# Kernel optimization log

Measured on AMD Instinct MI355X. Metric: run time of the kernel, lower is better.

Reference implementation:

```python
import jax, jax.numpy as jnp
import numpy as np

S, T, B = 120, 10, 128          # sentence len, word len, batch
E, HW, HS = 80, 75, 700         # embedding, word-GRU hidden, sentence-GRU hidden
V = 30000                       # vocab size


def gru_scan(x, Wih, Whh, bih, bhh):
    """Single-direction GRU (PyTorch gate math). x: [T, N, in] -> (ys [T,N,H], h_T [N,H])."""
    H = Whh.shape[-1]
    xw = jnp.einsum('tni,gi->tng', x, Wih) + bih  # precompute input gates [T,N,3H]

    def step(h, xw_t):
        gh = h @ Whh.T + bhh
        r = jax.nn.sigmoid(xw_t[..., :H] + gh[..., :H])
        z = jax.nn.sigmoid(xw_t[..., H:2 * H] + gh[..., H:2 * H])
        n = jnp.tanh(xw_t[..., 2 * H:] + r * gh[..., 2 * H:])
        h_new = (1.0 - z) * n + z * h
        return h_new, h_new

    h0 = jnp.zeros((x.shape[1], H), x.dtype)
    hT, ys = jax.lax.scan(step, h0, xw)
    return ys, hT


def bigru_layer(x, Wih, Whh, bih, bhh):
    """Bidirectional GRU layer; params have leading dir axis [2,...]."""
    yf, hf = gru_scan(x, Wih[0], Whh[0], bih[0], bhh[0])
    yb, hb = gru_scan(x[::-1], Wih[1], Whh[1], bih[1], bhh[1])
    y = jnp.concatenate([yf, yb[::-1]], axis=-1)
    return y, hf, hb


def setup_inputs() -> dict:
    key = jax.random.key(0)
    ks = iter(jax.random.split(key, 40))

    def p(shape):
        return jax.random.normal(next(ks), shape, jnp.float32) * 0.05

    inp = {'x': jax.random.randint(next(ks), (S, T, B), 0, V)}
    inp['emb'] = p((V, E))
    # word encoder: 2-layer bi-GRU, layer0 in=E, layer1 in=2*HW
    inp['we_Wih0'] = p((2, 3 * HW, E)); inp['we_Whh0'] = p((2, 3 * HW, HW))
    inp['we_bih0'] = p((2, 3 * HW)); inp['we_bhh0'] = p((2, 3 * HW))
    inp['we_Wih1'] = p((2, 3 * HW, 2 * HW)); inp['we_Whh1'] = p((2, 3 * HW, HW))
    inp['we_bih1'] = p((2, 3 * HW)); inp['we_bhh1'] = p((2, 3 * HW))
    # sentence encoder: 2-layer bi-GRU, layer0 in=4*HW=300, layer1 in=2*HS
    inp['se_Wih0'] = p((2, 3 * HS, 4 * HW)); inp['se_Whh0'] = p((2, 3 * HS, HS))
    inp['se_bih0'] = p((2, 3 * HS)); inp['se_bhh0'] = p((2, 3 * HS))
    inp['se_Wih1'] = p((2, 3 * HS, 2 * HS)); inp['se_Whh1'] = p((2, 3 * HS, HS))
    inp['se_bih1'] = p((2, 3 * HS)); inp['se_bhh1'] = p((2, 3 * HS))
    return inp


def reference(x, emb,
              we_Wih0, we_Whh0, we_bih0, we_bhh0,
              we_Wih1, we_Whh1, we_bih1, we_bhh1,
              se_Wih0, se_Whh0, se_bih0, se_bhh0,
              se_Wih1, se_Whh1, se_bih1, se_bhh1):
    # Fold the python loop over 120 sentence positions into the batch:
    # x [S,T,B] -> [T, S*B]
    xt = jnp.transpose(x, (1, 0, 2)).reshape(T, S * B)
    xe = emb[xt]  # [T, S*B, E]
    y0, hf0, hb0 = bigru_layer(xe, we_Wih0, we_Whh0, we_bih0, we_bhh0)
    _, hf1, hb1 = bigru_layer(y0, we_Wih1, we_Whh1, we_bih1, we_bhh1)
    # torch h stacking: [l0_fwd, l0_bwd, l1_fwd, l1_bwd] concat on feature dim
    words = jnp.concatenate([hf0, hb0, hf1, hb1], axis=-1)  # [S*B, 4*HW]
    words = words.reshape(S, B, 4 * HW)
    y0s, sf0, sb0 = bigru_layer(words, se_Wih0, se_Whh0, se_bih0, se_bhh0)
    _, sf1, sb1 = bigru_layer(y0s, se_Wih1, se_Whh1, se_bih1, se_bhh1)
    h = jnp.concatenate([sf0, sb0, sf1, sb1], axis=-1)[None]  # [1, B, 4*HS]
    return h
```

## Files before the change

kernel.cpp:

```cpp
#include <hip/hip_runtime.h>
#include <hip/hip_bf16.h>

typedef __hip_bfloat16 bf16;
typedef __attribute__((ext_vector_type(8))) short bf16x8;
typedef __attribute__((ext_vector_type(4))) short bf16x4;
typedef __attribute__((ext_vector_type(4))) float f32x4;

__device__ __forceinline__ void stC(float* p, float v) { *p = v; }
__device__ __forceinline__ void stC(bf16* p, float v)  { *p = __float2bfloat16(v); }

__device__ __forceinline__ short f2s(float f) {
    bf16 b = __float2bfloat16(f);
    return __builtin_bit_cast(short, b);
}

__device__ __forceinline__ void gload16(const void* gp, void* lp) {
    __builtin_amdgcn_global_load_lds(
        (const __attribute__((address_space(1))) void*)gp,
        (__attribute__((address_space(3))) void*)lp, 16, 0, 0);
}

__device__ __forceinline__ float sigm(float x) {
    x = fminf(fmaxf(x, -40.f), 40.f);
    return 1.f / (1.f + expf(-x));
}
__device__ __forceinline__ float tanh_s(float x) {
    x = fminf(fmaxf(x, -20.f), 20.f);
    float e = expf(2.f * x);
    return 1.f - 2.f / (e + 1.f);
}

__device__ __forceinline__ bf16x8 ld8(const bf16* p) {
    return *reinterpret_cast<const bf16x8*>(p);
}
__device__ __forceinline__ bf16x8 ld8(const float* p) {
    const float4 f0 = *reinterpret_cast<const float4*>(p);
    const float4 f1 = *reinterpret_cast<const float4*>(p + 4);
    bf16x8 v;
    v[0] = f2s(f0.x); v[1] = f2s(f0.y); v[2] = f2s(f0.z); v[3] = f2s(f0.w);
    v[4] = f2s(f1.x); v[5] = f2s(f1.y); v[6] = f2s(f1.z); v[7] = f2s(f1.w);
    return v;
}
__device__ __forceinline__ bf16x8 ld8_8B(const bf16* p) {
    bf16x4 lo = *reinterpret_cast<const bf16x4*>(p);
    bf16x4 hi = *reinterpret_cast<const bf16x4*>(p + 4);
    bf16x8 v;
    v[0] = lo[0]; v[1] = lo[1]; v[2] = lo[2]; v[3] = lo[3];
    v[4] = hi[0]; v[5] = hi[1]; v[6] = hi[2]; v[7] = hi[3];
    return v;
}

__global__ void f2b(const float* __restrict__ src, bf16* __restrict__ dst, long n) {
    long i = (long)blockIdx.x * 256 + threadIdx.x;
    if (i < n) dst[i] = __float2bfloat16(src[i]);
}
__global__ void f2bpad(const float* __restrict__ src, bf16* __restrict__ dst,
                       int rows, int Ks, int Kd) {
    long i = (long)blockIdx.x * 256 + threadIdx.x;
    if (i >= (long)rows * Kd) return;
    int c = i % Kd; long r = i / Kd;
    dst[i] = __float2bfloat16(c < Ks ? src[r * Ks + c] : 0.f);
}
__global__ void f2bremap(const float* __restrict__ src, bf16* __restrict__ dst, int rows) {
    long i = (long)blockIdx.x * 256 + threadIdx.x;
    if (i >= (long)rows * 160) return;
    int c = i % 160; long r = i / 160;
    float v = 0.f;
    if (c < 75) v = src[r * 150 + c];
    else if (c >= 80 && c < 155) v = src[r * 150 + c - 5];
    dst[i] = __float2bfloat16(v);
}

#define MBM 128
#define MBN 64
#define MLD 40

__global__ __launch_bounds__(256) void gemm_mfma(
    const float* __restrict__ A, long sAd,
    const float* __restrict__ W, long sWd,
    bf16* __restrict__ C, long sCd,
    int M, int Nc, int K)
{
    __shared__ bf16 As[MBM * MLD];
    __shared__ bf16 Ws[MBN * MLD];
    const int d = blockIdx.z;
    A += (long)d * sAd; W += (long)d * sWd; C += (long)d * sCd;
    const int m0 = blockIdx.y * MBM;
    const int n0 = blockIdx.x * MBN;
    const int tid = threadIdx.x;
    const int w = tid >> 6, l = tid & 63;
    const int lr = l & 15, lq = l >> 4;

    f32x4 acc[2][4] = {};
    for (int k0 = 0; k0 < K; k0 += 32) {
#pragma unroll
        for (int i = 0; i < 2; ++i) {
            int u = tid + i * 256;
            int r = u >> 2, kk = (u & 3) * 8;
            bf16x8 v = {};
            if (m0 + r < M && k0 + kk < K)
                v = ld8(A + (long)(m0 + r) * K + k0 + kk);
            *reinterpret_cast<bf16x8*>(&As[r * MLD + kk]) = v;
        }
        {
            int r = tid >> 2, kk = (tid & 3) * 8;
            bf16x8 v = {};
            if (n0 + r < Nc && k0 + kk < K)
                v = ld8(W + (long)(n0 + r) * K + k0 + kk);
            *reinterpret_cast<bf16x8*>(&Ws[r * MLD + kk]) = v;
        }
        __syncthreads();
        bf16x8 af[2], bw[4];
        af[0] = *reinterpret_cast<const bf16x8*>(&As[(w * 32 + lr) * MLD + lq * 8]);
        af[1] = *reinterpret_cast<const bf16x8*>(&As[(w * 32 + 16 + lr) * MLD + lq * 8]);
#pragma unroll
        for (int ni = 0; ni < 4; ++ni)
            bw[ni] = *reinterpret_cast<const bf16x8*>(&Ws[(ni * 16 + lr) * MLD + lq * 8]);
#pragma unroll
        for (int mi = 0; mi < 2; ++mi)
#pragma unroll
            for (int ni = 0; ni < 4; ++ni)
                acc[mi][ni] = __builtin_amdgcn_mfma_f32_16x16x32_bf16(
                    af[mi], bw[ni], acc[mi][ni], 0, 0, 0);
        __syncthreads();
    }
#pragma unroll
    for (int mi = 0; mi < 2; ++mi)
#pragma unroll
        for (int reg = 0; reg < 4; ++reg) {
            int m = m0 + w * 32 + mi * 16 + lq * 4 + reg;
            if (m >= M) continue;
#pragma unroll
            for (int ni = 0; ni < 4; ++ni) {
                int n = n0 + ni * 16 + lr;
                if (n < Nc) stC(&C[(long)m * Nc + n], acc[mi][ni][reg]);
            }
        }
}

__global__ __launch_bounds__(256) void gemm_bt(
    const bf16* __restrict__ A, long sAd,
    const bf16* __restrict__ W, long sWd,
    bf16* __restrict__ C, long sCd,
    int M, int Nc, int KP)
{
    __shared__ bf16 As[128 * 64];
    __shared__ bf16 Ws[128 * 64];
    const int d = blockIdx.z;
    A += (long)d * sAd; W += (long)d * sWd; C += (long)d * sCd;
    const int nx = (Nc + 127) >> 7, ny = M >> 7;
    int id = blockIdx.x;
    int band = id / (8 * ny);
    int rr = id - band * 8 * ny;
    int bwd = nx - band * 8; if (bwd > 8) bwd = 8;
    const int bx = band * 8 + rr % bwd;
    const int by = rr / bwd;
    const int m0 = by << 7;
    const int n0 = bx << 7;
    const int tid = threadIdx.x;
    const int w = tid >> 6, l = tid & 63;
    const int lr = l & 15, lq = l >> 4;

    const int sr = tid >> 3;
    const int sg = tid & 7;
    const bf16x8 z8 = {};
    bf16x8 ra[4], rb[4];
    auto stage = [&](int k0) {
        const bool kin = (k0 + sg * 8) < KP;
#pragma unroll
        for (int i = 0; i < 4; ++i)
            ra[i] = kin ? ld8(A + (long)(m0 + sr + i * 32) * KP + k0 + sg * 8) : z8;
#pragma unroll
        for (int i = 0; i < 4; ++i)
            rb[i] = kin ? ld8(W + (long)(n0 + sr + i * 32) * KP + k0 + sg * 8) : z8;
    };

    f32x4 acc[2][8] = {};
    stage(0);
    for (int k0 = 0; k0 < KP; k0 += 64) {
#pragma unroll
        for (int i = 0; i < 4; ++i) {
            const int r = sr + i * 32;
            const int g = sg ^ (r & 7);
            *reinterpret_cast<bf16x8*>(&As[r * 64 + g * 8]) = ra[i];
            *reinterpret_cast<bf16x8*>(&Ws[r * 64 + g * 8]) = rb[i];
        }
        __syncthreads();
        if (k0 + 64 < KP) stage(k0 + 64);
#pragma unroll
        for (int ks = 0; ks < 2; ++ks) {
            const int gb = ks * 4 + lq;
            bf16x8 af[2], bw8[8];
#pragma unroll
            for (int mi = 0; mi < 2; ++mi) {
                const int r = w * 32 + mi * 16 + lr;
                af[mi] = *reinterpret_cast<const bf16x8*>(
                    &As[r * 64 + (gb ^ (r & 7)) * 8]);
            }
#pragma unroll
            for (int ni = 0; ni < 8; ++ni) {
                const int r = ni * 16 + lr;
                bw8[ni] = *reinterpret_cast<const bf16x8*>(
                    &Ws[r * 64 + (gb ^ (r & 7)) * 8]);
            }
#pragma unroll
            for (int mi = 0; mi < 2; ++mi)
#pragma unroll
                for (int ni = 0; ni < 8; ++ni)
                    acc[mi][ni] = __builtin_amdgcn_mfma_f32_16x16x32_bf16(
                        af[mi], bw8[ni], acc[mi][ni], 0, 0, 0);
        }
        __syncthreads();
    }
#pragma unroll
    for (int mi = 0; mi < 2; ++mi)
#pragma unroll
        for (int reg = 0; reg < 4; ++reg) {
            int m = m0 + w * 32 + mi * 16 + lq * 4 + reg;
#pragma unroll
            for (int ni = 0; ni < 8; ++ni) {
                int n = n0 + ni * 16 + lr;
                if (n < Nc) C[(long)m * Nc + n] = __float2bfloat16(acc[mi][ni][reg]);
            }
        }
}

#define NKS 22
#define HBPE (2 * 128 * 700)

struct StepJob {
    const bf16* Whh;
    const bf16* xw;
    const float* bih;
    const float* bhh;
    float* h;
    const bf16* hr;
    bf16* hw;
    bf16* y;
    const bf16* zb;
    int te0, te1;
    int tl0, tl1;
};

__global__ __launch_bounds__(512) void gru_step_sent2(StepJob ja, StepJob jb, int Cbuf)
{
    extern __shared__ bf16 Wlds[];
    const StepJob J = blockIdx.y ? jb : ja;
    const int jt = blockIdx.x, d = blockIdx.z;
    const int tid = threadIdx.x;
    const int w = tid >> 6, l = tid & 63;
    const int lr = l & 15, lq = l >> 4;
    const int j0c = jt * 16;
    const int jcol = j0c + lr;
    const bool jok = jcol < 700;

    const bf16* Wd = J.Whh + (long)d * 2100 * 700;
    {
        const int row = j0c + lr;
        const int kof = lq * 8;
#pragma unroll
        for (int i = 0; i < 9; ++i) {
            const int issue = w + i * 8;
            if (issue < 66) {
                const int g = issue % 3;
                const int kk = issue / 3;
                const bf16* src = (row < 700)
                    ? Wd + (long)(g * 700 + row) * 700 + kk * 32 + kof
                    : J.zb;
                gload16(src, &Wlds[(long)issue * 512]);
            }
        }
    }

    const int arow = w * 16 + lr;
    const bf16* Ab = J.hr + ((long)d * 128 + arow) * 700;
    bf16x8 areg[NKS];
#pragma unroll
    for (int kk = 0; kk < NKS; ++kk) {
        const int kb = kk * 32 + lq * 8;
        if (kb + 8 <= 700) {
            areg[kk] = ld8_8B(Ab + kb);
        } else {
            bf16x8 v = {};
            bf16x4 lo = *reinterpret_cast<const bf16x4*>(Ab + kb);
            v[0] = lo[0]; v[1] = lo[1]; v[2] = lo[2]; v[3] = lo[3];
            areg[kk] = v;
        }
    }

    const int te = d ? J.te1 : J.te0;
    const int tl = d ? J.tl1 : J.tl0;
    const bf16* xbase = J.xw + ((long)d * Cbuf + tl) * 128 * 2100;
    bf16 xg[3][4];
#pragma unroll
    for (int reg = 0; reg < 4; ++reg) {
        const int m = w * 16 + lq * 4 + reg;
        const bf16* xp = xbase + (long)m * 2100 + jcol;
#pragma unroll
        for (int g = 0; g < 3; ++g) xg[g][reg] = jok ? xp[g * 700] : bf16(0.f);
    }
    const int jc = jok ? jcol : 699;
    const float bir = J.bih[d * 2100 + jc];
    const float biz = J.bih[d * 2100 + 700 + jc];
    const float bin = J.bih[d * 2100 + 1400 + jc];
    const float bhr = J.bhh[d * 2100 + jc];
    const float bhz = J.bhh[d * 2100 + 700 + jc];
    const float bhn = J.bhh[d * 2100 + 1400 + jc];

    __syncthreads();

    f32x4 acc[3] = {};
#pragma unroll
    for (int kk = 0; kk < NKS; ++kk)
#pragma unroll
        for (int g = 0; g < 3; ++g) {
            bf16x8 b = *reinterpret_cast<const bf16x8*>(&Wlds[((kk * 3 + g) * 64 + l) * 8]);
            acc[g] = __builtin_amdgcn_mfma_f32_16x16x32_bf16(areg[kk], b, acc[g], 0, 0, 0);
        }

    if (jok) {
#pragma unroll
        for (int reg = 0; reg < 4; ++reg) {
            const int m = w * 16 + lq * 4 + reg;
            float r  = sigm((float)xg[0][reg] + bir + acc[0][reg] + bhr);
            float z  = sigm((float)xg[1][reg] + biz + acc[1][reg] + bhz);
            float nn = tanh_s((float)xg[2][reg] + bin + r * (acc[2][reg] + bhn));
            const long hidx = ((long)d * 128 + m) * 700 + jcol;
            const float hnew = (1.f - z) * nn + z * J.h[hidx];
            J.h[hidx] = hnew;
            J.hw[hidx] = __float2bfloat16(hnew);
            if (J.y) J.y[((long)te * 128 + m) * 1408 + (long)d * 700 + jcol] =
                         __float2bfloat16(hnew);
        }
    }
}

#define WNW 15360

__global__ __launch_bounds__(512) void gru_word0_fused(
    const int* __restrict__ x,
    const bf16* __restrict__ embW,
    const bf16* __restrict__ Whh,
    const float* __restrict__ bih,
    const float* __restrict__ bhh,
    const bf16* __restrict__ hr,
    bf16* __restrict__ hw,
    float* __restrict__ h,
    bf16* __restrict__ y,
    int T, int k)
{
    __shared__ bf16 Wl[3 * 3 * 64 * 8];
    const int jt = blockIdx.x, mt = blockIdx.y, d = blockIdx.z;
    const int tid = threadIdx.x;
    const int w = tid >> 6, l = tid & 63;
    const int lr = l & 15, lq = l >> 4;
    const int j0c = jt * 16, jcol = j0c + lr;
    const bool jok = jcol < 75;
    const int t_eff = d ? (T - 1 - k) : k;

    const int na = mt * 128 + w * 16 + lr;
    const bf16* Ab = hr + ((long)d * WNW + na) * 96;
    bf16x8 areg[3];
#pragma unroll
    for (int kk = 0; kk < 3; ++kk) areg[kk] = ld8(Ab + kk * 32 + lq * 8);

    float xg[3][4];
#pragma unroll
    for (int reg = 0; reg < 4; ++reg) {
        const int m = mt * 128 + w * 16 + lq * 4 + reg;
        const int s = m >> 7, b = m & 127;
        int tok = x[(s * T + t_eff) * 128 + b];
        tok = max(0, min(29999, tok));
        const bf16* ep = embW + ((long)d * 30000 + tok) * 225;
#pragma unroll
        for (int g = 0; g < 3; ++g)
            xg[g][reg] = jok ? (float)ep[g * 75 + jcol] : 0.f;
    }
    const int jc = jok ? jcol : 74;
    const float bir = bih[d*225+jc], biz = bih[d*225+75+jc], bin = bih[d*225+150+jc];
    const float bhr = bhh[d*225+jc], bhz = bhh[d*225+75+jc], bhn = bhh[d*225+150+jc];

    const bf16* Wd = Whh + (long)d * 225 * 80;
    for (int u = tid; u < 3 * 3 * 64; u += 512) {
        int lane = u & 63;
        int g = (u >> 6) % 3;
        int kk = u / 192;
        int row = j0c + (lane & 15);
        int kb = kk * 32 + (lane >> 4) * 8;
        bf16x8 v = {};
        if (row < 75 && kb < 80) v = ld8_8B(Wd + (long)(g * 75 + row) * 80 + kb);
        *reinterpret_cast<bf16x8*>(&Wl[u * 8]) = v;
    }
    __syncthreads();

    f32x4 acc[3] = {};
#pragma unroll
    for (int kk = 0; kk < 3; ++kk)
#pragma unroll
        for (int g = 0; g < 3; ++g) {
            bf16x8 b8 = *reinterpret_cast<const bf16x8*>(&Wl[((kk*3+g)*64 + l)*8]);
            acc[g] = __builtin_amdgcn_mfma_f32_16x16x32_bf16(areg[kk], b8, acc[g], 0, 0, 0);
        }

    if (jok) {
#pragma unroll
        for (int reg = 0; reg < 4; ++reg) {
            const int m = mt * 128 + w * 16 + lq * 4 + reg;
            float r  = sigm(xg[0][reg] + bir + acc[0][reg] + bhr);
            float z  = sigm(xg[1][reg] + biz + acc[1][reg] + bhz);
            float nn = tanh_s(xg[2][reg] + bin + r * (acc[2][reg] + bhn));
            const long hif = ((long)d * WNW + m) * 75 + jcol;
            const float hnew = (1.f - z) * nn + z * h[hif];
            h[hif] = hnew;
            hw[((long)d * WNW + m) * 96 + jcol] = __float2bfloat16(hnew);
            y[((long)t_eff * WNW + m) * 160 + d * 80 + jcol] = __float2bfloat16(hnew);
        }
    }
}

__global__ __launch_bounds__(512) void gru_word1_fused(
    const bf16* __restrict__ y0,
    const bf16* __restrict__ Wih,
    const bf16* __restrict__ Whh,
    const float* __restrict__ bih,
    const float* __restrict__ bhh,
    const bf16* __restrict__ hr,
    bf16* __restrict__ hw,
    float* __restrict__ h,
    int T, int k)
{
    __shared__ bf16 Wl[8 * 3 * 64 * 8];
    const int jt = blockIdx.x, mt = blockIdx.y, d = blockIdx.z;
    const int tid = threadIdx.x;
    const int w = tid >> 6, l = tid & 63;
    const int lr = l & 15, lq = l >> 4;
    const int j0c = jt * 16, jcol = j0c + lr;
    const bool jok = jcol < 75;
    const int t_eff = d ? (T - 1 - k) : k;

    const int na = mt * 128 + w * 16 + lr;
    const bf16* A1 = y0 + ((long)t_eff * WNW + na) * 160;
    bf16x8 a1[5];
#pragma unroll
    for (int kk = 0; kk < 5; ++kk) a1[kk] = ld8(A1 + kk * 32 + lq * 8);
    const bf16* A2 = hr + ((long)d * WNW + na) * 96;
    bf16x8 a2[3];
#pragma unroll
    for (int kk = 0; kk < 3; ++kk) a2[kk] = ld8(A2 + kk * 32 + lq * 8);

    const int jc = jok ? jcol : 74;
    const float bir = bih[d*225+jc], biz = bih[d*225+75+jc], bin = bih[d*225+150+jc];
    const float bhr = bhh[d*225+jc], bhz = bhh[d*225+75+jc], bhn = bhh[d*225+150+jc];

    const bf16* Wx = Wih + (long)d * 225 * 160;
    for (int u = tid; u < 960; u += 512) {
        int lane = u & 63;
        int g = (u >> 6) % 3;
        int kk = u / 192;
        int row = j0c + (lane & 15);
        int kb = kk * 32 + (lane >> 4) * 8;
        bf16x8 v = {};
        if (row < 75) v = ld8(Wx + (long)(g * 75 + row) * 160 + kb);
        *reinterpret_cast<bf16x8*>(&Wl[u * 8]) = v;
    }
    const bf16* Wd = Whh + (long)d * 225 * 80;
    for (int u = tid; u < 576; u += 512) {
        int lane = u & 63;
        int g = (u >> 6) % 3;
        int kk = u / 192;
        int row = j0c + (lane & 15);
        int kb = kk * 32 + (lane >> 4) * 8;
        bf16x8 v = {};
        if (row < 75 && kb < 80) v = ld8_8B(Wd + (long)(g * 75 + row) * 80 + kb);
        *reinterpret_cast<bf16x8*>(&Wl[(960 + u) * 8]) = v;
    }
    __syncthreads();

    f32x4 ax[3] = {}, ah[3] = {};
#pragma unroll
    for (int kk = 0; kk < 5; ++kk)
#pragma unroll
        for (int g = 0; g < 3; ++g) {
            bf16x8 b8 = *reinterpret_cast<const bf16x8*>(&Wl[((kk*3+g)*64 + l)*8]);
            ax[g] = __builtin_amdgcn_mfma_f32_16x16x32_bf16(a1[kk], b8, ax[g], 0, 0, 0);
        }
#pragma unroll
    for (int kk = 0; kk < 3; ++kk)
#pragma unroll
        for (int g = 0; g < 3; ++g) {
            bf16x8 b8 = *reinterpret_cast<const bf16x8*>(&Wl[(960 + (kk*3+g)*64 + l)*8]);
            ah[g] = __builtin_amdgcn_mfma_f32_16x16x32_bf16(a2[kk], b8, ah[g], 0, 0, 0);
        }

    if (jok) {
#pragma unroll
        for (int reg = 0; reg < 4; ++reg) {
            const int m = mt * 128 + w * 16 + lq * 4 + reg;
            float r  = sigm(ax[0][reg] + bir + ah[0][reg] + bhr);
            float z  = sigm(ax[1][reg] + biz + ah[1][reg] + bhz);
            float nn = tanh_s(ax[2][reg] + bin + r * (ah[2][reg] + bhn));
            const long hif = ((long)d * WNW + m) * 75 + jcol;
            const float hnew = (1.f - z) * nn + z * h[hif];
            h[hif] = hnew;
            hw[((long)d * WNW + m) * 96 + jcol] = __float2bfloat16(hnew);
        }
    }
}

template <typename OT>
__global__ void concat4(const float* __restrict__ ha, const float* __restrict__ hb,
                        OT* __restrict__ out, int N, int H, int OS)
{
    long idx = (long)blockIdx.x * 256 + threadIdx.x;
    int C4 = 4 * H;
    if (idx >= (long)N * C4) return;
    int c = idx % C4;
    long n = idx / C4;
    int blk = c / H, j = c % H;
    const float* src = (blk < 2) ? ha : hb;
    int dd = blk & 1;
    stC(&out[n * (long)OS + c], src[((long)dd * N + n) * H + j]);
}

extern "C" void kernel_launch(void* const* d_in, const int* in_sizes, int n_in,
                              void* d_out, int out_size, void* d_ws, size_t ws_size,
                              hipStream_t stream)
{
    const int S = 120, T = 10, B = 128, E = 80, HW = 75, HS = 700, V = 30000;
    const int Nw = S * B;
    const int Gw = 3 * HW;
    const int Gs = 3 * HS;
    (void)in_sizes; (void)n_in; (void)out_size; (void)ws_size;

    const int*   x       = (const int*)d_in[0];
    const float* emb     = (const float*)d_in[1];
    const float* we_Wih0 = (const float*)d_in[2],  *we_Whh0 = (const float*)d_in[3];
    const float* we_bih0 = (const float*)d_in[4],  *we_bhh0 = (const float*)d_in[5];
    const float* we_Wih1 = (const float*)d_in[6],  *we_Whh1 = (const float*)d_in[7];
    const float* we_bih1 = (const float*)d_in[8],  *we_bhh1 = (const float*)d_in[9];
    const float* se_Wih0 = (const float*)d_in[10], *se_Whh0 = (const float*)d_in[11];
    const float* se_bih0 = (const float*)d_in[12], *se_bhh0 = (const float*)d_in[13];
    const float* se_Wih1 = (const float*)d_in[14], *se_Whh1 = (const float*)d_in[15];
    const float* se_bih1 = (const float*)d_in[16], *se_bhh1 = (const float*)d_in[17];

    char* ws = (char*)d_ws;
    const size_t oP1 = 9830400;
    const size_t oP2 = oP1 + 49152000;
    const size_t oP3 = oP2 + 43008000;
    const size_t r4  = 30516480;
    const size_t total = oP3 + r4 + 256;

    bf16*  words  = (bf16*)ws;
    bf16*  y0w    = (bf16*)(ws + oP1);
    bf16*  embW   = (bf16*)(ws + oP2);
    float* h_w0   = (float*)(ws + oP3);
    float* h_w1   = (float*)(ws + oP3 + 9216000);
    bf16*  pingW  = (bf16*)(ws + oP3 + 18432000);
    bf16*  Whh0bw = (bf16*)(ws + oP3 + 30228480);
    bf16*  Whh1bw = (bf16*)(ws + oP3 + 30300480);
    bf16*  Wih1pw = (bf16*)(ws + oP3 + 30372480);
    const long PWE = 2L * Nw * 96;
    bf16*  y0s    = (bf16*)(ws + oP1);
    bf16*  bufL0  = (bf16*)(ws + oP2);
    bf16*  bufL1  = (bf16*)(ws + oP2 + 21504000);
    bf16*  Whh0b  = (bf16*)(ws + oP3);
    bf16*  Whh1b  = (bf16*)(ws + oP3 + 5880000);
    bf16*  hbf0   = (bf16*)(ws + oP3 + 11760000);
    bf16*  hbf1   = (bf16*)(ws + oP3 + 12476800);
    float* h_s0   = (float*)(ws + oP3 + 13193600);
    float* h_s1   = (float*)(ws + oP3 + 13910400);
    bf16*  Wih0p  = (bf16*)(ws + oP3 + 14627200);
    bf16*  Wih1p  = (bf16*)(ws + oP3 + 17412480);
    const bf16* zscr = (const bf16*)(ws + oP3 + r4);

    hipMemsetAsync(ws, 0, oP2, stream);
    hipMemsetAsync(ws + oP3, 0, r4 + 256, stream);

    gemm_mfma<<<dim3((Gw + MBN - 1) / MBN, (V + MBM - 1) / MBM, 2), 256, 0, stream>>>(
        emb, 0, we_Wih0, (long)Gw * E, embW, (long)V * Gw, V, Gw, E);
    for (int d = 0; d < 2; ++d) {
        f2bpad<<<(225 * 80 + 255) / 256, 256, 0, stream>>>(
            we_Whh0 + (long)d * 225 * 75, Whh0bw + (long)d * 225 * 80, 225, 75, 80);
        f2bpad<<<(225 * 80 + 255) / 256, 256, 0, stream>>>(
            we_Whh1 + (long)d * 225 * 75, Whh1bw + (long)d * 225 * 80, 225, 75, 80);
        f2bremap<<<(225 * 160 + 255) / 256, 256, 0, stream>>>(
            we_Wih1 + (long)d * 225 * 150, Wih1pw + (long)d * 225 * 160, 225);
    }
    dim3 wgrid(5, Nw / 128, 2);
    for (int k = 0; k < T; ++k) {
        int p = k & 1;
        gru_word0_fused<<<wgrid, 512, 0, stream>>>(
            x, embW, Whh0bw, we_bih0, we_bhh0,
            pingW + (long)p * PWE, pingW + (long)(p ^ 1) * PWE, h_w0, y0w, T, k);
    }
    hipMemsetAsync(pingW, 0, 11796480, stream);
    for (int k = 0; k < T; ++k) {
        int p = k & 1;
        gru_word1_fused<<<wgrid, 512, 0, stream>>>(
            y0w, Wih1pw, Whh1bw, we_bih1, we_bhh1,
            pingW + (long)p * PWE, pingW + (long)(p ^ 1) * PWE, h_w1, T, k);
    }
    {
        long tot = (long)Nw * 4 * HW;
        concat4<bf16><<<(tot + 255) / 256, 256, 0, stream>>>(h_w0, h_w1, words, Nw, HW, 320);
    }

    {
        long nwh = 2LL * Gs * HS;
        f2b<<<(nwh + 255) / 256, 256, 0, stream>>>(se_Whh0, Whh0b, nwh);
        f2b<<<(nwh + 255) / 256, 256, 0, stream>>>(se_Whh1, Whh1b, nwh);
        for (int d = 0; d < 2; ++d) {
            f2bpad<<<((long)2100 * 320 + 255) / 256, 256, 0, stream>>>(
                se_Wih0 + (long)d * 2100 * 300, Wih0p + (long)d * 2176 * 320, 2100, 300, 320);
            f2bpad<<<((long)2100 * 1408 + 255) / 256, 256, 0, stream>>>(
                se_Wih1 + (long)d * 2100 * 1400, Wih1p + (long)d * 2176 * 1408, 2100, 1400, 1408);
        }
    }
    hipMemsetAsync(ws + oP3 + 11760000, 0, 2867200, stream);

    const unsigned ldsBytes = 67584;
    const int C2 = 20, NC = 6;
    const int nblk = ((Gs + 127) / 128) * ((C2 * B) / 128);

    for (int t = 0; t <= NC; ++t) {
        if (t < NC) {
            int tb0 = t * C2, tb1 = S - t * C2 - C2;
            gemm_bt<<<dim3(nblk, 1, 2), 256, 0, stream>>>(
                words + (long)tb0 * B * 320, (long)(tb1 - tb0) * B * 320,
                Wih0p, (long)2176 * 320,
                bufL0, (long)C2 * B * Gs, C2 * B, Gs, 320);
        }
        if (t >= 1) {
            int c = t - 1, tb0 = c * C2, tb1 = S - c * C2 - C2;
            gemm_bt<<<dim3(nblk, 1, 2), 256, 0, stream>>>(
                y0s + (long)tb0 * B * 1408, (long)(tb1 - tb0) * B * 1408,
                Wih1p, (long)2176 * 1408,
                bufL1, (long)C2 * B * Gs, C2 * B, Gs, 1408);
        }
        for (int i = 0; i < C2; ++i) {
            StepJob jobs[2]; int nj = 0;
            if (t < NC) {
                int k = t * C2 + i;
                StepJob J;
                J.Whh = Whh0b; J.xw = bufL0; J.bih = se_bih0; J.bhh = se_bhh0;
                J.h = h_s0;
                int p = k & 1;
                J.hr = hbf0 + (long)p * HBPE; J.hw = hbf0 + (long)(p ^ 1) * HBPE;
                J.y = y0s; J.zb = zscr;
                J.te0 = k; J.te1 = S - 1 - k; J.tl0 = i; J.tl1 = C2 - 1 - i;
                jobs[nj++] = J;
            }
            if (t >= 1) {
                int k = (t - 1) * C2 + i;
                StepJob J;
                J.Whh = Whh1b; J.xw = bufL1; J.bih = se_bih1; J.bhh = se_bhh1;
                J.h = h_s1;
                int p = k & 1;
                J.hr = hbf1 + (long)p * HBPE; J.hw = hbf1 + (long)(p ^ 1) * HBPE;
                J.y = nullptr; J.zb = zscr;
                J.te0 = k; J.te1 = S - 1 - k; J.tl0 = i; J.tl1 = C2 - 1 - i;
                jobs[nj++] = J;
            }
            if (nj == 1) jobs[1] = jobs[0];
            gru_step_sent2<<<dim3(44, nj, 2), 512, ldsBytes, stream>>>(
                jobs[0], jobs[1], C2);
        }
    }

    {
        long tot = (long)B * 4 * HS;
        concat4<float><<<(tot + 255) / 256, 256, 0, stream>>>(
            h_s0, h_s1, (float*)d_out, B, HS, 4 * HS);
    }
}
```

Measured before the change: 3.100 ms.

## Process all column tiles per block in word GRU kernels

The word-level GRU step kernels drop the column-tile grid dimension. Each block now loops over all five 16-column tiles, so the hidden-state A fragments, token ids and y0 fragments are loaded once and reused across tiles. The whole Whh (and Wih for layer 1) is staged into LDS per block, which needs about 120KB of dynamic shared memory for layer 1. The grid shrinks from 1200 to 240 blocks, and each block does five tiles of work serially, so latency hiding and occupancy may suffer in exchange for fewer redundant loads.

Result: faster. 2.936 ms (-5.3%).

```diff
diff --git a/kernel.cpp b/kernel.cpp
--- a/kernel.cpp
+++ b/kernel.cpp
@@ -349,13 +349,11 @@
     bf16* __restrict__ y,
     int T, int k)
 {
-    __shared__ bf16 Wl[3 * 3 * 64 * 8];
-    const int jt = blockIdx.x, mt = blockIdx.y, d = blockIdx.z;
+    __shared__ bf16 Wl[45 * 64 * 8];
+    const int mt = blockIdx.x, d = blockIdx.y;
     const int tid = threadIdx.x;
     const int w = tid >> 6, l = tid & 63;
     const int lr = l & 15, lq = l >> 4;
-    const int j0c = jt * 16, jcol = j0c + lr;
-    const bool jok = jcol < 75;
     const int t_eff = d ? (T - 1 - k) : k;
 
     const int na = mt * 128 + w * 16 + lr;
@@ -364,28 +362,23 @@
 #pragma unroll
     for (int kk = 0; kk < 3; ++kk) areg[kk] = ld8(Ab + kk * 32 + lq * 8);
 
-    float xg[3][4];
+    int toks[4];
 #pragma unroll
     for (int reg = 0; reg < 4; ++reg) {
         const int m = mt * 128 + w * 16 + lq * 4 + reg;
         const int s = m >> 7, b = m & 127;
         int tok = x[(s * T + t_eff) * 128 + b];
-        tok = max(0, min(29999, tok));
-        const bf16* ep = embW + ((long)d * 30000 + tok) * 225;
-#pragma unroll
-        for (int g = 0; g < 3; ++g)
-            xg[g][reg] = jok ? (float)ep[g * 75 + jcol] : 0.f;
-    }
-    const int jc = jok ? jcol : 74;
-    const float bir = bih[d*225+jc], biz = bih[d*225+75+jc], bin = bih[d*225+150+jc];
-    const float bhr = bhh[d*225+jc], bhz = bhh[d*225+75+jc], bhn = bhh[d*225+150+jc];
+        toks[reg] = max(0, min(29999, tok));
+    }
 
     const bf16* Wd = Whh + (long)d * 225 * 80;
-    for (int u = tid; u < 3 * 3 * 64; u += 512) {
+    for (int u = tid; u < 45 * 64; u += 512) {
         int lane = u & 63;
-        int g = (u >> 6) % 3;
-        int kk = u / 192;
-        int row = j0c + (lane & 15);
+        int c = u >> 6;
+        int jt = c / 9;
+        int rem = c - jt * 9;
+        int kk = rem / 3, g = rem - kk * 3;
+        int row = jt * 16 + (lane & 15);
         int kb = kk * 32 + (lane >> 4) * 8;
         bf16x8 v = {};
         if (row < 75 && kb < 80) v = ld8_8B(Wd + (long)(g * 75 + row) * 80 + kb);
@@ -393,22 +386,33 @@
     }
     __syncthreads();
 
-    f32x4 acc[3] = {};
-#pragma unroll
-    for (int kk = 0; kk < 3; ++kk)
-#pragma unroll
-        for (int g = 0; g < 3; ++g) {
-            bf16x8 b8 = *reinterpret_cast<const bf16x8*>(&Wl[((kk*3+g)*64 + l)*8]);
-            acc[g] = __builtin_amdgcn_mfma_f32_16x16x32_bf16(areg[kk], b8, acc[g], 0, 0, 0);
-        }
-
-    if (jok) {
+    const bf16* eb = embW + (long)d * 30000 * 225;
+    for (int jt = 0; jt < 5; ++jt) {
+        const int jcol = jt * 16 + lr;
+        const bool jok = jcol < 75;
+        f32x4 acc[3] = {};
+#pragma unroll
+        for (int kk = 0; kk < 3; ++kk)
+#pragma unroll
+            for (int g = 0; g < 3; ++g) {
+                bf16x8 b8 = *reinterpret_cast<const bf16x8*>(
+                    &Wl[((jt * 9 + kk * 3 + g) * 64 + l) * 8]);
+                acc[g] = __builtin_amdgcn_mfma_f32_16x16x32_bf16(
+                    areg[kk], b8, acc[g], 0, 0, 0);
+            }
+        if (!jok) continue;
+        const float bir = bih[d*225+jcol], biz = bih[d*225+75+jcol], bin = bih[d*225+150+jcol];
+        const float bhr = bhh[d*225+jcol], bhz = bhh[d*225+75+jcol], bhn = bhh[d*225+150+jcol];
 #pragma unroll
         for (int reg = 0; reg < 4; ++reg) {
             const int m = mt * 128 + w * 16 + lq * 4 + reg;
-            float r  = sigm(xg[0][reg] + bir + acc[0][reg] + bhr);
-            float z  = sigm(xg[1][reg] + biz + acc[1][reg] + bhz);
-            float nn = tanh_s(xg[2][reg] + bin + r * (acc[2][reg] + bhn));
+            const bf16* ep = eb + (long)toks[reg] * 225;
+            float xr = (float)ep[jcol];
+            float xz = (float)ep[75 + jcol];
+            float xn = (float)ep[150 + jcol];
+            float r  = sigm(xr + bir + acc[0][reg] + bhr);
+            float z  = sigm(xz + biz + acc[1][reg] + bhz);
+            float nn = tanh_s(xn + bin + r * (acc[2][reg] + bhn));
             const long hif = ((long)d * WNW + m) * 75 + jcol;
             const float hnew = (1.f - z) * nn + z * h[hif];
             h[hif] = hnew;
@@ -429,13 +433,11 @@
     float* __restrict__ h,
     int T, int k)
 {
-    __shared__ bf16 Wl[8 * 3 * 64 * 8];
-    const int jt = blockIdx.x, mt = blockIdx.y, d = blockIdx.z;
+    extern __shared__ bf16 Wl1[];
+    const int mt = blockIdx.x, d = blockIdx.y;
     const int tid = threadIdx.x;
     const int w = tid >> 6, l = tid & 63;
     const int lr = l & 15, lq = l >> 4;
-    const int j0c = jt * 16, jcol = j0c + lr;
-    const bool jok = jcol < 75;
     const int t_eff = d ? (T - 1 - k) : k;
 
     const int na = mt * 128 + w * 16 + lr;
@@ -448,51 +450,59 @@
 #pragma unroll
     for (int kk = 0; kk < 3; ++kk) a2[kk] = ld8(A2 + kk * 32 + lq * 8);
 
-    const int jc = jok ? jcol : 74;
-    const float bir = bih[d*225+jc], biz = bih[d*225+75+jc], bin = bih[d*225+150+jc];
-    const float bhr = bhh[d*225+jc], bhz = bhh[d*225+75+jc], bhn = bhh[d*225+150+jc];
-
     const bf16* Wx = Wih + (long)d * 225 * 160;
-    for (int u = tid; u < 960; u += 512) {
+    for (int u = tid; u < 75 * 64; u += 512) {
         int lane = u & 63;
-        int g = (u >> 6) % 3;
-        int kk = u / 192;
-        int row = j0c + (lane & 15);
+        int c = u >> 6;
+        int jt = c / 15;
+        int rem = c - jt * 15;
+        int kk = rem / 3, g = rem - kk * 3;
+        int row = jt * 16 + (lane & 15);
         int kb = kk * 32 + (lane >> 4) * 8;
         bf16x8 v = {};
         if (row < 75) v = ld8(Wx + (long)(g * 75 + row) * 160 + kb);
-        *reinterpret_cast<bf16x8*>(&Wl[u * 8]) = v;
+        *reinterpret_cast<bf16x8*>(&Wl1[u * 8]) = v;
     }
     const bf16* Wd = Whh + (long)d * 225 * 80;
-    for (int u = tid; u < 576; u += 512) {
+    for (int u = tid; u < 45 * 64; u += 512) {
         int lane = u & 63;
-        int g = (u >> 6) % 3;
-        int kk = u / 192;
-        int row = j0c + (lane & 15);
+        int c = u >> 6;
+        int jt = c / 9;
+        int rem = c - jt * 9;
+        int kk = rem / 3, g = rem - kk * 3;
+        int row = jt * 16 + (lane & 15);
         int kb = kk * 32 + (lane >> 4) * 8;
         bf16x8 v = {};
         if (row < 75 && kb < 80) v = ld8_8B(Wd + (long)(g * 75 + row) * 80 + kb);
-        *reinterpret_cast<bf16x8*>(&Wl[(960 + u) * 8]) = v;
+        *reinterpret_cast<bf16x8*>(&Wl1[(75 * 64 + u) * 8]) = v;
     }
     __syncthreads();
 
-    f32x4 ax[3] = {}, ah[3] = {};
-#pragma unroll
-    for (int kk = 0; kk < 5; ++kk)
-#pragma unroll
-        for (int g = 0; g < 3; ++g) {
-            bf16x8 b8 = *reinterpret_cast<const bf16x8*>(&Wl[((kk*3+g)*64 + l)*8]);
-            ax[g] = __builtin_amdgcn_mfma_f32_16x16x32_bf16(a1[kk], b8, ax[g], 0, 0, 0);
-        }
-#pragma unroll
-    for (int kk = 0; kk < 3; ++kk)
-#pragma unroll
-        for (int g = 0; g < 3; ++g) {
-            bf16x8 b8 = *reinterpret_cast<const bf16x8*>(&Wl[(960 + (kk*3+g)*64 + l)*8]);
-            ah[g] = __builtin_amdgcn_mfma_f32_16x16x32_bf16(a2[kk], b8, ah[g], 0, 0, 0);
-        }
-
-    if (jok) {
+    for (int jt = 0; jt < 5; ++jt) {
+        const int jcol = jt * 16 + lr;
+        const bool jok = jcol < 75;
+        f32x4 ax[3] = {}, ah[3] = {};
+#pragma unroll
+        for (int kk = 0; kk < 5; ++kk)
+#pragma unroll
+            for (int g = 0; g < 3; ++g) {
+                bf16x8 b8 = *reinterpret_cast<const bf16x8*>(
+                    &Wl1[((jt * 15 + kk * 3 + g) * 64 + l) * 8]);
+                ax[g] = __builtin_amdgcn_mfma_f32_16x16x32_bf16(
+                    a1[kk], b8, ax[g], 0, 0, 0);
+            }
+#pragma unroll
+        for (int kk = 0; kk < 3; ++kk)
+#pragma unroll
+            for (int g = 0; g < 3; ++g) {
+                bf16x8 b8 = *reinterpret_cast<const bf16x8*>(
+                    &Wl1[(75 * 64 + (jt * 9 + kk * 3 + g) * 64 + l) * 8]);
+                ah[g] = __builtin_amdgcn_mfma_f32_16x16x32_bf16(
+                    a2[kk], b8, ah[g], 0, 0, 0);
+            }
+        if (!jok) continue;
+        const float bir = bih[d*225+jcol], biz = bih[d*225+75+jcol], bin = bih[d*225+150+jcol];
+        const float bhr = bhh[d*225+jcol], bhz = bhh[d*225+75+jcol], bhn = bhh[d*225+150+jcol];
 #pragma unroll
         for (int reg = 0; reg < 4; ++reg) {
             const int m = mt * 128 + w * 16 + lq * 4 + reg;
@@ -586,7 +596,7 @@
         f2bremap<<<(225 * 160 + 255) / 256, 256, 0, stream>>>(
             we_Wih1 + (long)d * 225 * 150, Wih1pw + (long)d * 225 * 160, 225);
     }
-    dim3 wgrid(5, Nw / 128, 2);
+    dim3 wgrid(Nw / 128, 2);
     for (int k = 0; k < T; ++k) {
         int p = k & 1;
         gru_word0_fused<<<wgrid, 512, 0, stream>>>(
@@ -596,7 +606,7 @@
     hipMemsetAsync(pingW, 0, 11796480, stream);
     for (int k = 0; k < T; ++k) {
         int p = k & 1;
-        gru_word1_fused<<<wgrid, 512, 0, stream>>>(
+        gru_word1_fused<<<wgrid, 512, 122880, stream>>>(
             y0w, Wih1pw, Whh1bw, we_bih1, we_bhh1,
             pingW + (long)p * PWE, pingW + (long)(p ^ 1) * PWE, h_w1, T, k);
     }
```
